# Optimization experiments

Hardware: AMD Instinct MI355X
Metric: run time of the kernel (lower is better)

Reference implementation:

```python
import jax, jax.numpy as jnp
import numpy as np
import math

N_HEADS = 16
ROPE_THETA = 10000.0


def _rope_cos_sin(seqlen, head_dim, theta=ROPE_THETA):
    # freqs_cis = polar(1, outer(t, 1/theta^(2i/d))) -> return cos, sin parts
    inv = 1.0 / (theta ** (jnp.arange(0, head_dim, 2, dtype=jnp.float32) / head_dim))
    t = jnp.arange(seqlen, dtype=jnp.float32)
    freqs = t[:, None] * inv[None, :]          # [S, hd/2]
    return jnp.cos(freqs), jnp.sin(freqs)


def _apply_rope(x, cos, sin):
    # x: [B, S, H, hd]; treat consecutive pairs as complex, rotate by e^{i*freq}
    B, S, H, hd = x.shape
    x2 = x.astype(jnp.float32).reshape(B, S, H, hd // 2, 2)
    xr, xi = x2[..., 0], x2[..., 1]
    c = cos[None, :, None, :]
    s = sin[None, :, None, :]
    out_r = xr * c - xi * s
    out_i = xr * s + xi * c
    return jnp.stack([out_r, out_i], axis=-1).reshape(B, S, H, hd).astype(x.dtype)


def setup_inputs() -> dict:
    key = jax.random.key(0)
    ks = jax.random.split(key, 5)
    dim = 2048
    B, S = 2, 2048
    scale = 1.0 / math.sqrt(dim)
    x = jax.random.normal(ks[0], (B, S, dim), dtype=jnp.float32)
    wq = jax.random.normal(ks[1], (dim, dim), dtype=jnp.float32) * scale
    wk = jax.random.normal(ks[2], (dim, dim), dtype=jnp.float32) * scale
    wv = jax.random.normal(ks[3], (dim, dim), dtype=jnp.float32) * scale
    wo = jax.random.normal(ks[4], (dim, dim), dtype=jnp.float32) * scale
    return {"x": x, "wq": wq, "wk": wk, "wv": wv, "wo": wo}


def reference(x, wq, wk, wv, wo):
    B, S, D = x.shape
    H = N_HEADS
    hd = D // H
    # nn.Linear(bias=False): y = x @ W.T
    q = (x @ wq.T).reshape(B, S, H, hd)
    k = (x @ wk.T).reshape(B, S, H, hd)
    v = (x @ wv.T).reshape(B, S, H, hd)
    cos, sin = _rope_cos_sin(S, hd)
    q = _apply_rope(q, cos, sin)
    k = _apply_rope(k, cos, sin)
    attn = jnp.einsum('bthd,bThd->bhtT', q, k) / jnp.sqrt(jnp.float32(hd))
    attn = jax.nn.softmax(attn, axis=-1)
    out = jnp.einsum('bhtT,bThd->bthd', attn, v).reshape(B, S, D)
    return out @ wo.T
```

## Files before the change

kernel.cpp:

```cpp
#include <hip/hip_runtime.h>
#include <math.h>

typedef unsigned short u16;
typedef __bf16 bf16x8 __attribute__((ext_vector_type(8)));
typedef short s16x4 __attribute__((ext_vector_type(4)));
typedef short s16x8 __attribute__((ext_vector_type(8)));
typedef float f32x4 __attribute__((ext_vector_type(4)));

#define B_ 2
#define S_ 2048
#define D_ 2048
#define H_ 16
#define HD_ 128
#define M_ 4096
#define N3_ 6144

#define AS1(p) ((__attribute__((address_space(1))) void*)(void*)(p))
#define AS3(p) ((__attribute__((address_space(3))) void*)(p))
#define GLD16(g, l) __builtin_amdgcn_global_load_lds(AS1(g), AS3(l), 16, 0, 0)

__device__ __forceinline__ u16 f2bf(float f) {
  unsigned u = __float_as_uint(f);
  return (u16)((u + 0x7FFFu + ((u >> 16) & 1u)) >> 16);
}
__device__ __forceinline__ float bf2f(u16 v) {
  return __uint_as_float(((unsigned)v) << 16);
}

__global__ void cvt5_k(const float* __restrict__ x, const float* __restrict__ wq,
                       const float* __restrict__ wk, const float* __restrict__ wv,
                       const float* __restrict__ wo, u16* __restrict__ xb,
                       u16* __restrict__ wqkvb, u16* __restrict__ wob) {
  int y = blockIdx.y;
  const float* s;
  u16* d;
  int n4;
  if (y == 0) {
    s = x; d = xb; n4 = M_ * D_ / 4;
  } else {
    s = (y == 1) ? wq : (y == 2) ? wk : (y == 3) ? wv : wo;
    d = (y == 4) ? wob : wqkvb + (size_t)(y - 1) * D_ * D_;
    n4 = D_ * D_ / 4;
  }
  int i = blockIdx.x * 256 + threadIdx.x;
  if (i >= n4) return;
  float4 v = ((const float4*)s)[i];
  ushort4 o;
  o.x = f2bf(v.x); o.y = f2bf(v.y); o.z = f2bf(v.z); o.w = f2bf(v.w);
  ((ushort4*)d)[i] = o;
}

__global__ void rope_tab_k(float2* __restrict__ tab) {
  int t = blockIdx.x * 256 + threadIdx.x;
  if (t >= S_ * 64) return;
  int s = t >> 6, i = t & 63;
  double inv = exp2(-(double)i * (13.287712379549449 / 64.0));
  double fr = (double)s * inv;
  double sv, cv;
  sincos(fr, &sv, &cv);
  tab[t] = make_float2((float)cv, (float)sv);
}

template <typename OT>
__global__ __launch_bounds__(256) void gemm_bt_k(const u16* __restrict__ A,
                                                 const u16* __restrict__ B,
                                                 OT* __restrict__ C,
                                                 int M, int N, int K) {
  __shared__ alignas(16) u16 As[128 * 32];
  __shared__ alignas(16) u16 Bs[128 * 32];
  const int tid = threadIdx.x;
  const int wave = tid >> 6, lane = tid & 63;
  const int quad = lane >> 4, l16 = lane & 15;
  const int m0 = blockIdx.y * 128, n0 = blockIdx.x * 128;
  const int wm = (wave >> 1) * 64, wn = (wave & 1) * 64;
  const u16* Ag = A + (size_t)m0 * K;
  const u16* Bg = B + (size_t)n0 * K;
  f32x4 acc[4][4] = {};
  const int c0 = tid, c1 = tid + 256;
  const int r0 = c0 >> 2, k0b = (c0 & 3) * 8;
  const int r1 = c1 >> 2, k1b = (c1 & 3) * 8;
  u16* la0 = As + (size_t)(wave * 64) * 8;
  u16* la1 = As + (size_t)(256 + wave * 64) * 8;
  u16* lb0 = Bs + (size_t)(wave * 64) * 8;
  u16* lb1 = Bs + (size_t)(256 + wave * 64) * 8;
  for (int kt = 0; kt < K; kt += 32) {
    GLD16(Ag + (size_t)r0 * K + kt + k0b, la0);
    GLD16(Ag + (size_t)r1 * K + kt + k1b, la1);
    GLD16(Bg + (size_t)r0 * K + kt + k0b, lb0);
    GLD16(Bg + (size_t)r1 * K + kt + k1b, lb1);
    __syncthreads();
    bf16x8 af[4], bfr[4];
#pragma unroll
    for (int i = 0; i < 4; ++i)
      af[i] = *(const bf16x8*)&As[(wm + i * 16 + l16) * 32 + quad * 8];
#pragma unroll
    for (int j = 0; j < 4; ++j)
      bfr[j] = *(const bf16x8*)&Bs[(wn + j * 16 + l16) * 32 + quad * 8];
#pragma unroll
    for (int i = 0; i < 4; ++i)
#pragma unroll
      for (int j = 0; j < 4; ++j)
        acc[i][j] = __builtin_amdgcn_mfma_f32_16x16x32_bf16(af[i], bfr[j], acc[i][j], 0, 0, 0);
    __syncthreads();
  }
#pragma unroll
  for (int i = 0; i < 4; ++i) {
#pragma unroll
    for (int j = 0; j < 4; ++j) {
      int n = n0 + wn + j * 16 + l16;
#pragma unroll
      for (int r = 0; r < 4; ++r) {
        int m = m0 + wm + i * 16 + quad * 4 + r;
        if constexpr (sizeof(OT) == 4)
          C[(size_t)m * N + n] = acc[i][j][r];
        else
          C[(size_t)m * N + n] = f2bf(acc[i][j][r]);
      }
    }
  }
}

__global__ void rope_k(const u16* __restrict__ qkv, const float2* __restrict__ tab,
                       u16* __restrict__ Qr, u16* __restrict__ Kr) {
  int t = blockIdx.x * 256 + threadIdx.x;
  int m = t >> 10;
  int h = (t >> 6) & 15;
  int i = t & 63;
  int s = m & (S_ - 1);
  int b = m >> 11;
  float2 cs = tab[(s << 6) | i];
  const u16* qp = qkv + (size_t)m * N3_ + h * HD_ + 2 * i;
  ushort2 qv = *(const ushort2*)qp;
  ushort2 kv = *(const ushort2*)(qp + D_);
  float qr = bf2f(qv.x), qi = bf2f(qv.y);
  float kr = bf2f(kv.x), ki = bf2f(kv.y);
  ushort2 qo, ko;
  qo.x = f2bf(qr * cs.x - qi * cs.y);
  qo.y = f2bf(qr * cs.y + qi * cs.x);
  ko.x = f2bf(kr * cs.x - ki * cs.y);
  ko.y = f2bf(kr * cs.y + ki * cs.x);
  size_t o = ((size_t)(b * H_ + h) * S_ + s) * HD_ + 2 * i;
  *(ushort2*)(Qr + o) = qo;
  *(ushort2*)(Kr + o) = ko;
}

__global__ __launch_bounds__(256) void vperm_k(const u16* __restrict__ qkv,
                                               u16* __restrict__ Vp) {
  int bh = blockIdx.y;
  int b = bh >> 4, h = bh & 15;
  int t = blockIdx.x * 256 + threadIdx.x;
  int d = t & 127, g = t >> 7;
  const u16* src = qkv + ((size_t)(b * S_ + 4 * g)) * N3_ + 2 * D_ + h * HD_ + d;
  ushort4 o;
  o.x = src[0];
  o.y = src[N3_];
  o.z = src[2 * N3_];
  o.w = src[3 * N3_];
  *(ushort4*)(Vp + (size_t)bh * S_ * HD_ + (size_t)t * 4) = o;
}

#if __has_builtin(__builtin_amdgcn_mfma_f32_16x16x16bf16_1k)
#define HAS_MFMA16 1
#endif

__global__ __launch_bounds__(256, 2) void flash_k(const u16* __restrict__ Q,
                                                  const u16* __restrict__ Kc,
                                                  const u16* __restrict__ Vp,
                                                  u16* __restrict__ O) {
  __shared__ alignas(16) u16 sm[32768];
  const int tid = threadIdx.x;
  const int wave = tid >> 6, lane = tid & 63;
  const int quad = lane >> 4, l16 = lane & 15;
  const int qt = blockIdx.x, bh = blockIdx.y;
  const int b = bh >> 4, h = bh & 15;
  const u16* vbase_g = Vp + (size_t)bh * S_ * HD_;

#pragma unroll
  for (int i = 0; i < 8; ++i) {
    int c = i * 256 + tid, row = c >> 4, jl = c & 15;
    int gj = (jl & 8) | ((jl ^ row) & 7);
    GLD16(Q + ((size_t)bh * S_ + qt * 128 + row) * HD_ + gj * 8,
          sm + (size_t)(i * 256 + wave * 64) * 8);
  }
#pragma unroll
  for (int i = 0; i < 4; ++i) {
    int c = i * 256 + tid, row = c >> 4, jl = c & 15;
    int gj = (jl & 8) | ((jl ^ row) & 7);
    GLD16(Kc + ((size_t)bh * S_ + row) * HD_ + gj * 8,
          sm + 16384 + (size_t)(i * 256 + wave * 64) * 8);
    GLD16(vbase_g + (size_t)(i * 256 + tid) * 8,
          sm + 24576 + (size_t)(i * 256 + wave * 64) * 8);
  }
  __syncthreads();

  bf16x8 qf[2][4];
#pragma unroll
  for (int qs = 0; qs < 2; ++qs) {
    int row = wave * 32 + qs * 16 + l16;
#pragma unroll
    for (int dk = 0; dk < 4; ++dk) {
      int c = dk * 4 + quad, pj = (c & 8) | ((c ^ row) & 7);
      qf[qs][dk] = *(const bf16x8*)&sm[row * 128 + pj * 8];
    }
  }
  __syncthreads();

  f32x4 acco[2][8] = {};
  f32x4 accl[2] = {};
  const float SCL = 0.08838834764831845f * 1.4426950408889634f;
#ifdef HAS_MFMA16
  const s16x4 ones = {(short)0x3F80, (short)0x3F80, (short)0x3F80, (short)0x3F80};
#else
  union { s16x8 s; bf16x8 b; } onesu;
  onesu.s = (s16x8){(short)0x3F80, (short)0x3F80, (short)0x3F80, (short)0x3F80,
                    (short)0x3F80, (short)0x3F80, (short)0x3F80, (short)0x3F80};
#endif

#pragma unroll 1
  for (int kt = 0; kt < 32; ++kt) {
    u16* cb = sm + ((kt & 1) ? 0 : 16384);
    u16* nb = sm + ((kt & 1) ? 16384 : 0);
    if (kt < 31) {
      const u16* vg = vbase_g + (size_t)(kt + 1) * 8192;
#pragma unroll
      for (int i = 0; i < 4; ++i) {
        int c = i * 256 + tid, row = c >> 4, jl = c & 15;
        int gj = (jl & 8) | ((jl ^ row) & 7);
        GLD16(Kc + ((size_t)bh * S_ + (kt + 1) * 64 + row) * HD_ + gj * 8,
              nb + (size_t)(i * 256 + wave * 64) * 8);
        GLD16(vg + (size_t)(i * 256 + tid) * 8,
              nb + 8192 + (size_t)(i * 256 + wave * 64) * 8);
      }
    }

    f32x4 sc[2][4] = {};
#pragma unroll
    for (int k4 = 0; k4 < 4; ++k4) {
      int row = k4 * 16 + l16;
#pragma unroll
      for (int dk = 0; dk < 4; ++dk) {
        int c = dk * 4 + quad, pj = (c & 8) | ((c ^ row) & 7);
        bf16x8 kf = *(const bf16x8*)&cb[row * 128 + pj * 8];
        sc[0][k4] = __builtin_amdgcn_mfma_f32_16x16x32_bf16(kf, qf[0][dk], sc[0][k4], 0, 0, 0);
        sc[1][k4] = __builtin_amdgcn_mfma_f32_16x16x32_bf16(kf, qf[1][dk], sc[1][k4], 0, 0, 0);
      }
    }

#ifdef HAS_MFMA16
    s16x4 ap[2][4];
#else
    bf16x8 ap[2][4];
#endif
#pragma unroll
    for (int qs = 0; qs < 2; ++qs) {
#pragma unroll
      for (int k4 = 0; k4 < 4; ++k4) {
        f32x4 s = sc[qs][k4];
        u16 p0 = f2bf(__builtin_amdgcn_exp2f(s[0] * SCL));
        u16 p1 = f2bf(__builtin_amdgcn_exp2f(s[1] * SCL));
        u16 p2 = f2bf(__builtin_amdgcn_exp2f(s[2] * SCL));
        u16 p3 = f2bf(__builtin_amdgcn_exp2f(s[3] * SCL));
#ifdef HAS_MFMA16
        ap[qs][k4] = (s16x4){(short)p0, (short)p1, (short)p2, (short)p3};
#else
        union { s16x8 s8; bf16x8 b8; } u;
        u.s8 = (s16x8){(short)p0, (short)p1, (short)p2, (short)p3, 0, 0, 0, 0};
        ap[qs][k4] = u.b8;
#endif
      }
    }

#pragma unroll
    for (int ck = 0; ck < 4; ++ck) {
      int vb = 8192 + (ck * 4 + quad) * 512 + l16 * 4;
#pragma unroll
      for (int df = 0; df < 8; ++df) {
        s16x4 bv = *(const s16x4*)&cb[vb + df * 64];
#ifdef HAS_MFMA16
        acco[0][df] = __builtin_amdgcn_mfma_f32_16x16x16bf16_1k(ap[0][ck], bv, acco[0][df], 0, 0, 0);
        acco[1][df] = __builtin_amdgcn_mfma_f32_16x16x16bf16_1k(ap[1][ck], bv, acco[1][df], 0, 0, 0);
#else
        union { s16x8 s8; bf16x8 b8; } vbu;
        vbu.s8 = (s16x8){bv[0], bv[1], bv[2], bv[3], 0, 0, 0, 0};
        acco[0][df] = __builtin_amdgcn_mfma_f32_16x16x32_bf16(ap[0][ck], vbu.b8, acco[0][df], 0, 0, 0);
        acco[1][df] = __builtin_amdgcn_mfma_f32_16x16x32_bf16(ap[1][ck], vbu.b8, acco[1][df], 0, 0, 0);
#endif
      }
#ifdef HAS_MFMA16
      accl[0] = __builtin_amdgcn_mfma_f32_16x16x16bf16_1k(ones, ap[0][ck], accl[0], 0, 0, 0);
      accl[1] = __builtin_amdgcn_mfma_f32_16x16x16bf16_1k(ones, ap[1][ck], accl[1], 0, 0, 0);
#else
      accl[0] = __builtin_amdgcn_mfma_f32_16x16x32_bf16(onesu.b, ap[0][ck], accl[0], 0, 0, 0);
      accl[1] = __builtin_amdgcn_mfma_f32_16x16x32_bf16(onesu.b, ap[1][ck], accl[1], 0, 0, 0);
#endif
    }
    __syncthreads();
  }

#pragma unroll
  for (int qs = 0; qs < 2; ++qs) {
    float lv = accl[qs][0];
    float linv[4];
#pragma unroll
    for (int r = 0; r < 4; ++r) linv[r] = 1.0f / __shfl(lv, quad * 4 + r);
    int rowb = qt * 128 + wave * 32 + qs * 16 + quad * 4;
#pragma unroll
    for (int df = 0; df < 8; ++df) {
      int col = h * HD_ + df * 16 + l16;
#pragma unroll
      for (int r = 0; r < 4; ++r)
        O[((size_t)(b * S_ + rowb + r)) * D_ + col] = f2bf(acco[qs][df][r] * linv[r]);
    }
  }
}

extern "C" void kernel_launch(void* const* d_in, const int* in_sizes, int n_in,
                              void* d_out, int out_size, void* d_ws, size_t ws_size,
                              hipStream_t stream) {
  const float* x  = (const float*)d_in[0];
  const float* wq = (const float*)d_in[1];
  const float* wk = (const float*)d_in[2];
  const float* wv = (const float*)d_in[3];
  const float* wo = (const float*)d_in[4];

  size_t off = 0;
  char* ws = (char*)d_ws;
  u16* xb    = (u16*)(ws + off); off += (size_t)M_ * D_ * 2;
  u16* wqkvb = (u16*)(ws + off); off += (size_t)3 * D_ * D_ * 2;
  u16* wob   = (u16*)(ws + off); off += (size_t)D_ * D_ * 2;
  u16* qkv   = (u16*)(ws + off); off += (size_t)M_ * N3_ * 2;
  u16* Qr    = (u16*)(ws + off); off += (size_t)M_ * D_ * 2;
  u16* Kr    = (u16*)(ws + off); off += (size_t)M_ * D_ * 2;
  u16* Vp    = (u16*)(ws + off); off += (size_t)M_ * D_ * 2;
  float2* tab = (float2*)(ws + off); off += (size_t)S_ * 64 * sizeof(float2);
  u16* Ob = qkv;
  if (off > ws_size) return;

  cvt5_k<<<dim3(M_ * D_ / 4 / 256, 5), 256, 0, stream>>>(x, wq, wk, wv, wo, xb, wqkvb, wob);
  rope_tab_k<<<(S_ * 64) / 256, 256, 0, stream>>>(tab);
  gemm_bt_k<u16><<<dim3(N3_ / 128, M_ / 128), 256, 0, stream>>>(xb, wqkvb, qkv, M_, N3_, D_);
  rope_k<<<(M_ * H_ * 64) / 256, 256, 0, stream>>>(qkv, tab, Qr, Kr);
  vperm_k<<<dim3(S_ * HD_ / 4 / 256, B_ * H_), 256, 0, stream>>>(qkv, Vp);
  flash_k<<<dim3(S_ / 128, B_ * H_), 256, 0, stream>>>(Qr, Kr, Vp, Ob);
  gemm_bt_k<float><<<dim3(D_ / 128, M_ / 128), 256, 0, stream>>>(Ob, wob, (float*)d_out, M_, D_, D_);
}
```

Measured before the change: 440.1 us.

## Use 256x256-tile 8-wave GEMM with double-buffered LDS for QKV projection

Adds a new GEMM kernel with 256x256 output tiles, 512 threads and 64-wide K steps, and uses it for the QKV projection. Each step's four quadrant loads are interleaved with MFMA phases across a double-buffered 128KB LDS region, with XOR-swizzled LDS layout, s_setprio around the MFMA blocks, and an XCD-aware block remap. This aims to raise arithmetic intensity and overlap global-to-LDS traffic with compute compared with the 128x128 kernel. The cost is heavy LDS use, which limits occupancy, plus a complex barrier and waitcnt schedule that must stay correct. The output projection still uses the old kernel.

New measurement: 418.2 us. 1.05x faster.

```diff
diff --git a/kernel.cpp b/kernel.cpp
--- a/kernel.cpp
+++ b/kernel.cpp
@@ -59,6 +59,161 @@
   double sv, cv;
   sincos(fr, &sv, &cv);
   tab[t] = make_float2((float)cv, (float)sv);
+}
+
+template <typename OT>
+__global__ __launch_bounds__(512, 2) void gemm256_k(const u16* __restrict__ A,
+                                                    const u16* __restrict__ B,
+                                                    OT* __restrict__ C,
+                                                    int M, int N, int K) {
+  __shared__ alignas(16) u16 sm[65536];
+  const int tid = threadIdx.x;
+  const int wid = tid >> 6, lane = tid & 63;
+  const int quad = lane >> 4, l16 = lane & 15;
+  const int wr = wid >> 2, wc = wid & 3;
+
+  const int nby = M >> 8, nbx = N >> 8, nwg = nbx * nby;
+  int bid = blockIdx.x;
+  int wg = (nwg % 8 == 0) ? (bid % 8) * (nwg >> 3) + (bid >> 3) : bid;
+  const int m0 = (wg % nby) << 8, n0 = (wg / nby) << 8;
+
+  const int rr = tid >> 3;
+  const int sw8 = ((tid & 7) ^ (rr & 7)) * 8;
+  const int gb0 = (rr & 31) + ((rr & 32) << 1);
+  const u16* pA0_0 = A + (size_t)(m0 + rr) * K + sw8;
+  const u16* pA0_1 = A + (size_t)(m0 + 128 + rr) * K + sw8;
+  const u16* pA1_0 = A + (size_t)(m0 + 64 + rr) * K + sw8;
+  const u16* pA1_1 = A + (size_t)(m0 + 192 + rr) * K + sw8;
+  const u16* pB0_0 = B + (size_t)(n0 + gb0) * K + sw8;
+  const u16* pB0_1 = B + (size_t)(n0 + 128 + gb0) * K + sw8;
+  const u16* pB1_0 = B + (size_t)(n0 + 32 + gb0) * K + sw8;
+  const u16* pB1_1 = B + (size_t)(n0 + 160 + gb0) * K + sw8;
+  const int dst0 = wid * 64 * 8, dst1 = (512 + wid * 64) * 8;
+
+  const int pj0 = (quad ^ (l16 & 7)) * 8;
+  const int pj1 = ((4 + quad) ^ (l16 & 7)) * 8;
+
+  f32x4 acc[8][4] = {};
+  const int NT = K >> 6;
+
+  GLD16(pA0_0, sm + dst0);
+  GLD16(pA0_1, sm + dst1);
+  GLD16(pB0_0, sm + 32768 + dst0);
+  GLD16(pB0_1, sm + 32768 + dst1);
+  GLD16(pB1_0, sm + 32768 + 8192 + dst0);
+  GLD16(pB1_1, sm + 32768 + 8192 + dst1);
+  GLD16(pA1_0, sm + 8192 + dst0);
+  GLD16(pA1_1, sm + 8192 + dst1);
+  asm volatile("s_waitcnt vmcnt(4)" ::: "memory");
+  asm volatile("s_barrier" ::: "memory");
+
+  int koff = 0;
+#pragma unroll 1
+  for (int t = 0; t < NT; ++t) {
+    const int aB = (t & 1) * 16384, bB = 32768 + (t & 1) * 16384;
+    const int aN = ((t + 1) & 1) * 16384, bN = 32768 + ((t + 1) & 1) * 16384;
+    const bool pre = (t + 1 < NT);
+    const int kn = koff + 64;
+    bf16x8 a_[4][2], b_[4][2];
+
+#pragma unroll
+    for (int m = 0; m < 4; ++m) {
+      int rb = aB + (wr * 64 + m * 16 + l16) * 64;
+      a_[m][0] = *(const bf16x8*)&sm[rb + pj0];
+      a_[m][1] = *(const bf16x8*)&sm[rb + pj1];
+    }
+#pragma unroll
+    for (int n = 0; n < 2; ++n) {
+      int rb = bB + (wc * 32 + n * 16 + l16) * 64;
+      b_[n][0] = *(const bf16x8*)&sm[rb + pj0];
+      b_[n][1] = *(const bf16x8*)&sm[rb + pj1];
+    }
+    if (pre) { GLD16(pA0_0 + kn, sm + aN + dst0); GLD16(pA0_1 + kn, sm + aN + dst1); }
+    asm volatile("s_barrier" ::: "memory");
+    __builtin_amdgcn_s_setprio(1);
+#pragma unroll
+    for (int m = 0; m < 4; ++m)
+#pragma unroll
+      for (int n = 0; n < 2; ++n) {
+        acc[m][n] = __builtin_amdgcn_mfma_f32_16x16x32_bf16(a_[m][0], b_[n][0], acc[m][n], 0, 0, 0);
+        acc[m][n] = __builtin_amdgcn_mfma_f32_16x16x32_bf16(a_[m][1], b_[n][1], acc[m][n], 0, 0, 0);
+      }
+    __builtin_amdgcn_s_setprio(0);
+    if (pre) asm volatile("s_waitcnt vmcnt(4)" ::: "memory");
+    else     asm volatile("s_waitcnt vmcnt(0)" ::: "memory");
+    asm volatile("s_barrier" ::: "memory");
+
+#pragma unroll
+    for (int n = 0; n < 2; ++n) {
+      int rb = bB + (128 + wc * 32 + n * 16 + l16) * 64;
+      b_[2 + n][0] = *(const bf16x8*)&sm[rb + pj0];
+      b_[2 + n][1] = *(const bf16x8*)&sm[rb + pj1];
+    }
+    if (pre) { GLD16(pB0_0 + kn, sm + bN + dst0); GLD16(pB0_1 + kn, sm + bN + dst1); }
+    asm volatile("s_barrier" ::: "memory");
+    __builtin_amdgcn_s_setprio(1);
+#pragma unroll
+    for (int m = 0; m < 4; ++m)
+#pragma unroll
+      for (int n = 0; n < 2; ++n) {
+        acc[m][2 + n] = __builtin_amdgcn_mfma_f32_16x16x32_bf16(a_[m][0], b_[2 + n][0], acc[m][2 + n], 0, 0, 0);
+        acc[m][2 + n] = __builtin_amdgcn_mfma_f32_16x16x32_bf16(a_[m][1], b_[2 + n][1], acc[m][2 + n], 0, 0, 0);
+      }
+    __builtin_amdgcn_s_setprio(0);
+    if (pre) asm volatile("s_waitcnt vmcnt(4)" ::: "memory");
+    else     asm volatile("s_waitcnt vmcnt(0)" ::: "memory");
+    asm volatile("s_barrier" ::: "memory");
+
+#pragma unroll
+    for (int m = 0; m < 4; ++m) {
+      int rb = aB + (128 + wr * 64 + m * 16 + l16) * 64;
+      a_[m][0] = *(const bf16x8*)&sm[rb + pj0];
+      a_[m][1] = *(const bf16x8*)&sm[rb + pj1];
+    }
+    if (pre) { GLD16(pB1_0 + kn, sm + bN + 8192 + dst0); GLD16(pB1_1 + kn, sm + bN + 8192 + dst1); }
+    asm volatile("s_barrier" ::: "memory");
+    __builtin_amdgcn_s_setprio(1);
+#pragma unroll
+    for (int m = 0; m < 4; ++m)
+#pragma unroll
+      for (int n = 0; n < 2; ++n) {
+        acc[4 + m][n] = __builtin_amdgcn_mfma_f32_16x16x32_bf16(a_[m][0], b_[n][0], acc[4 + m][n], 0, 0, 0);
+        acc[4 + m][n] = __builtin_amdgcn_mfma_f32_16x16x32_bf16(a_[m][1], b_[n][1], acc[4 + m][n], 0, 0, 0);
+      }
+    __builtin_amdgcn_s_setprio(0);
+    asm volatile("s_barrier" ::: "memory");
+
+    if (pre) { GLD16(pA1_0 + kn, sm + aN + 8192 + dst0); GLD16(pA1_1 + kn, sm + aN + 8192 + dst1); }
+    asm volatile("s_barrier" ::: "memory");
+    __builtin_amdgcn_s_setprio(1);
+#pragma unroll
+    for (int m = 0; m < 4; ++m)
+#pragma unroll
+      for (int n = 0; n < 2; ++n) {
+        acc[4 + m][2 + n] = __builtin_amdgcn_mfma_f32_16x16x32_bf16(a_[m][0], b_[2 + n][0], acc[4 + m][2 + n], 0, 0, 0);
+        acc[4 + m][2 + n] = __builtin_amdgcn_mfma_f32_16x16x32_bf16(a_[m][1], b_[2 + n][1], acc[4 + m][2 + n], 0, 0, 0);
+      }
+    __builtin_amdgcn_s_setprio(0);
+    asm volatile("s_waitcnt vmcnt(4)" ::: "memory");
+    asm volatile("s_barrier" ::: "memory");
+    koff = kn;
+  }
+
+#pragma unroll
+  for (int m = 0; m < 8; ++m) {
+#pragma unroll
+    for (int n = 0; n < 4; ++n) {
+      int col = n0 + wc * 64 + n * 16 + l16;
+#pragma unroll
+      for (int r = 0; r < 4; ++r) {
+        int row = m0 + wr * 128 + m * 16 + quad * 4 + r;
+        if constexpr (sizeof(OT) == 4)
+          C[(size_t)row * N + col] = acc[m][n][r];
+        else
+          C[(size_t)row * N + col] = f2bf(acc[m][n][r]);
+      }
+    }
+  }
 }
 
 template <typename OT>
@@ -338,7 +493,7 @@
 
   cvt5_k<<<dim3(M_ * D_ / 4 / 256, 5), 256, 0, stream>>>(x, wq, wk, wv, wo, xb, wqkvb, wob);
   rope_tab_k<<<(S_ * 64) / 256, 256, 0, stream>>>(tab);
-  gemm_bt_k<u16><<<dim3(N3_ / 128, M_ / 128), 256, 0, stream>>>(xb, wqkvb, qkv, M_, N3_, D_);
+  gemm256_k<u16><<<(M_ / 256) * (N3_ / 256), 512, 0, stream>>>(xb, wqkvb, qkv, M_, N3_, D_);
   rope_k<<<(M_ * H_ * 64) / 256, 256, 0, stream>>>(qkv, tab, Qr, Kr);
   vperm_k<<<dim3(S_ * HD_ / 4 / 256, B_ * H_), 256, 0, stream>>>(qkv, Vp);
   flash_k<<<dim3(S_ / 128, B_ * H_), 256, 0, stream>>>(Qr, Kr, Vp, Ob);
```
